# Performance work log

Measured on AMD Instinct MI355X. Metric: run time of the kernel, lower is better.

Reference implementation:

```python
import jax, jax.numpy as jnp
import numpy as np

N = 4096        # number of nodes
C = 512         # in_features
L_LAT = 64      # L_latent
EPS = 0.25      # epsilon


def setup_inputs() -> dict:
    key = jax.random.key(0)
    ks = jax.random.split(key, 8)
    def lin(k, fan_in, shape):
        return (jax.random.normal(k, shape, jnp.float32) / np.float32(np.sqrt(fan_in)))
    x = jax.random.normal(ks[0], (N, C), jnp.float32)
    adj = jax.random.uniform(ks[1], (N, N), jnp.float32)  # dense nonneg kernel
    W_proj = lin(ks[2], C, (C, L_LAT)); b_proj = jnp.zeros((L_LAT,), jnp.float32)
    W_pi1 = lin(ks[3], L_LAT, (L_LAT, C)); b_pi1 = jnp.zeros((C,), jnp.float32)
    W_pi2 = lin(ks[4], C, (C, 1)); b_pi2 = jnp.zeros((1,), jnp.float32)
    W_f = lin(ks[5], C, (C, C)); b_f = jnp.zeros((C,), jnp.float32)
    dt = jnp.array([0.1], jnp.float32)
    return {"x": x, "adj": adj, "W_proj": W_proj, "b_proj": b_proj,
            "W_pi1": W_pi1, "b_pi1": b_pi1, "W_pi2": W_pi2, "b_pi2": b_pi2,
            "W_f": W_f, "b_f": b_f, "dt": dt}


def reference(x, adj, W_proj, b_proj, W_pi1, b_pi1, W_pi2, b_pi2, W_f, b_f, dt):
    # proj_list: x -> latent [n, L]
    z = x @ W_proj + b_proj
    # pi_list: Linear -> ReLU -> Linear -> Sigmoid, squeeze to [n]
    pi = jax.nn.sigmoid(jax.nn.relu(z @ W_pi1 + b_pi1) @ W_pi2 + b_pi2)[:, 0]
    # q_epsilon_tilde: row sums of the kernel
    q = adj.sum(axis=1)                       # [n]
    # K_tilde = K_epsilon @ diag(pi/q)  == column scaling
    K_tilde = adj * (pi / q)[None, :]         # [n, n]
    # D_tilde diagonal; torch.inverse of a diagonal == elementwise reciprocal
    d = K_tilde.sum(axis=1) + 1e-5            # [n]
    # target = relu(f(x)) with f = Linear(C, C)
    target = jax.nn.relu(x @ W_f + b_f)       # [n, C]
    # L @ target = (1/eps) * diag(1/d) @ K_tilde @ target - target
    Lt = (K_tilde @ target) / (EPS * d)[:, None] - target
    return target + dt[0] * Lt
```

## Files before the change

kernel.cpp:

```cpp
#include <hip/hip_runtime.h>
#include <hip/hip_bf16.h>

#define N_NODES 4096
#define C_DIM   512
#define L_DIM   64
#define SPLITS  4
#define KCHUNK  (N_NODES / SPLITS)

typedef unsigned short u16;
typedef unsigned int   u32;
using bf16x8 = __attribute__((ext_vector_type(8))) __bf16;
using u16x8  = __attribute__((ext_vector_type(8))) unsigned short;
using f32x4  = __attribute__((ext_vector_type(4))) float;

__device__ __forceinline__ float b2f(u16 u) {
    union { unsigned int i; float f; } v; v.i = ((unsigned int)u) << 16; return v.f;
}
__device__ __forceinline__ u16 f2b(float f) {
    unsigned int u = __float_as_uint(f);
    u += 0x7fff + ((u >> 16) & 1);
    return (u16)(u >> 16);
}
__device__ __forceinline__ void gload16(const void* g, void* l) {
    __builtin_amdgcn_global_load_lds((const __attribute__((address_space(1))) void*)g,
                                     (__attribute__((address_space(3))) void*)l,
                                     16, 0, 0);
}
__device__ __forceinline__ int detect_mode_inl(const u16* __restrict__ adj) {
    int m = 0;
#pragma unroll
    for (int i = 0; i < 64; ++i) m |= (adj[i] >= 0x8000) ? 1 : 0;
    return m;
}

#define OFF_MODE  0
#define OFF_DT    64
#define OFF_BIAS  1024
#define OFF_BP    4096
#define OFF_BP1   4608
#define OFF_WP2   8192
#define OFF_BP2   10240
#define OFF_Q     16384
#define OFF_S     32768
#define OFF_DV    49152
#define OFF_WPP   65536
#define OFF_WP1P  131072
#define OFF_WFT   196608
#define OFF_T     1048576
#define OFF_TST   9437184
#define OFF_XB    13631488
#define OFF_ADJB  17825792

__device__ __forceinline__ float ldin(const void* p, int i, int mode) {
    if (mode) return ((const float*)p)[i];
    return b2f(((const u16*)p)[i]);
}

__global__ __launch_bounds__(256) void k1_prep(const void* __restrict__ adj, const void* __restrict__ x,
        const void* Wp, const void* bp, const void* Wp1, const void* bp1,
        const void* Wp2, const void* bp2, const void* Wf, const void* bfc, const void* dt,
        int* __restrict__ modep,
        float* __restrict__ bp_f, float* __restrict__ bp1_f,
        float* __restrict__ Wp2_f, float* __restrict__ bp2_f,
        float* __restrict__ bias_f, float* __restrict__ dt_f,
        u32* __restrict__ WpP, u32* __restrict__ Wp1P,
        u16* __restrict__ adjb, float* __restrict__ q, u16* __restrict__ xb,
        u16* __restrict__ WfT) {
    __shared__ float tile[32][33];
    int bid = blockIdx.x, tid = threadIdx.x;
    int mode = detect_mode_inl((const u16*)adj);
    if (bid < 7) {
        if (bid == 0 && tid == 0) *modep = mode;
        int idx = bid * 256 + tid;
        if (idx < 64)           bp_f[idx]          = ldin(bp,  idx, mode);
        else if (idx < 576)     bp1_f[idx - 64]    = ldin(bp1, idx - 64, mode);
        else if (idx < 1088)    Wp2_f[idx - 576]   = ldin(Wp2, idx - 576, mode);
        else if (idx == 1088)   bp2_f[0]           = ldin(bp2, 0, mode);
        else if (idx < 1601)    bias_f[idx - 1089] = ldin(bfc, idx - 1089, mode);
        else if (idx == 1601)   dt_f[0]            = ldin(dt, 0, mode);
    } else if (bid < 2055) {
        if (mode == 0) return;
        int idx = (bid - 7) * 256 + tid;
        float4 v = ((const float4*)x)[idx];
        ushort4 o; o.x = f2b(v.x); o.y = f2b(v.y); o.z = f2b(v.z); o.w = f2b(v.w);
        ((ushort4*)xb)[idx] = o;
    } else if (bid < 3079) {
        int wave = tid >> 6, lane = tid & 63;
        int row = (bid - 2055) * 4 + wave;
        float acc = 0.f;
        if (mode) {
            const float4* rp = (const float4*)((const float*)adj + (size_t)row * N_NODES);
            ushort4* wp = (ushort4*)(adjb + (size_t)row * N_NODES);
#pragma unroll
            for (int it = 0; it < 16; ++it) {
                float4 v = rp[it * 64 + lane];
                acc += v.x + v.y + v.z + v.w;
                ushort4 o; o.x = f2b(v.x); o.y = f2b(v.y); o.z = f2b(v.z); o.w = f2b(v.w);
                wp[it * 64 + lane] = o;
            }
        } else {
            const u16x8* rp = (const u16x8*)((const u16*)adj + (size_t)row * N_NODES);
#pragma unroll
            for (int it = 0; it < 8; ++it) {
                u16x8 v = rp[it * 64 + lane];
#pragma unroll
                for (int e = 0; e < 8; ++e) acc += b2f(v[e]);
            }
        }
#pragma unroll
        for (int off = 32; off > 0; off >>= 1) acc += __shfl_down(acc, off);
        if (lane == 0) q[row] = acc;
    } else if (bid < 3335) {
        int g = bid - 3079;
        int tx = tid & 31, ty = tid >> 5;
        int x0 = (g & 15) * 32, y0 = (g >> 4) * 32;
        if (mode) {
            const float* src = (const float*)Wf;
#pragma unroll
            for (int r = ty; r < 32; r += 8) tile[r][tx] = src[(size_t)(y0 + r) * C_DIM + x0 + tx];
        } else {
            const u16* src = (const u16*)Wf;
#pragma unroll
            for (int r = ty; r < 32; r += 8) tile[r][tx] = b2f(src[(size_t)(y0 + r) * C_DIM + x0 + tx]);
        }
        __syncthreads();
#pragma unroll
        for (int r = ty; r < 32; r += 8)
            WfT[(size_t)(x0 + r) * C_DIM + y0 + tx] = f2b(tile[tx][r]);
    } else if (bid < 3399) {
        int idx = (bid - 3335) * 256 + tid;
        int k2i = idx >> 6, j = idx & 63;
        float a = ldin(Wp, (2 * k2i) * L_DIM + j, mode);
        float b = ldin(Wp, (2 * k2i + 1) * L_DIM + j, mode);
        WpP[idx] = (u32)f2b(a) | ((u32)f2b(b) << 16);
    } else {
        int idx = (bid - 3399) * 256 + tid;
        int jj2 = idx >> 9, m = idx & 511;
        float a = ldin(Wp1, (2 * jj2) * C_DIM + m, mode);
        float b = ldin(Wp1, (2 * jj2 + 1) * C_DIM + m, mode);
        Wp1P[idx] = (u32)f2b(a) | ((u32)f2b(b) << 16);
    }
}

__global__ __launch_bounds__(256) void k2_pi_gemm1(const void* __restrict__ xraw,
        const int* __restrict__ modep, const u16* __restrict__ xb, const u16* __restrict__ WfT,
        const u32* __restrict__ WpP, const u32* __restrict__ Wp1P,
        const float* __restrict__ bp_f,  const float* __restrict__ bp1_f,
        const float* __restrict__ Wp2_f, const float* __restrict__ bp2_f,
        const float* __restrict__ bias_f, const float* __restrict__ dt_f,
        const float* __restrict__ q, float* __restrict__ s, float* __restrict__ T,
        void* __restrict__ out, float* __restrict__ Pacc) {
    __shared__ __align__(16) char smem[26880];
    int bid = blockIdx.x, tid = threadIdx.x;
    int mode = *modep;
    if (bid < 512) {
        float (*sx)[C_DIM]      = (float(*)[C_DIM])smem;
        float (*red)[8][L_DIM]  = (float(*)[8][L_DIM])(smem + 16384);
        float (*sz)[L_DIM]      = (float(*)[L_DIM])(smem + 24576);
        float (*rw)[8]          = (float(*)[8])(smem + 26624);
        int i0 = bid * 8;
        const u16* xsrc = mode ? xb : (const u16*)xraw;
        const u16x8* xp = (const u16x8*)(xsrc + (size_t)i0 * C_DIM);
#pragma unroll
        for (int r = 0; r < 2; ++r) {
            u16x8 v = xp[tid + 256 * r];
            float* dstf = &sx[0][0] + (size_t)(tid + 256 * r) * 8;
#pragma unroll
            for (int e = 0; e < 8; ++e) dstf[e] = b2f(v[e]);
        }
        __syncthreads();
        int j = tid & 63, part = tid >> 6;
        float za[8];
#pragma unroll
        for (int n = 0; n < 8; ++n) za[n] = 0.f;
        const u32* wp = WpP + part * 4096 + j;
#pragma unroll 8
        for (int kk = 0; kk < 64; ++kk) {
            u32 w = wp[kk * 64];
            float wa = b2f((u16)(w & 0xFFFF)), wb = b2f((u16)(w >> 16));
            int k = part * 128 + kk * 2;
#pragma unroll
            for (int n = 0; n < 8; ++n) za[n] += sx[n][k] * wa + sx[n][k + 1] * wb;
        }
#pragma unroll
        for (int n = 0; n < 8; ++n) red[part][n][j] = za[n];
        __syncthreads();
#pragma unroll
        for (int r = 0; r < 2; ++r) {
            int idx = tid + r * 256; int n = idx >> 6, jj = idx & 63;
            sz[n][jj] = red[0][n][jj] + red[1][n][jj] + red[2][n][jj] + red[3][n][jj] + bp_f[jj];
        }
        __syncthreads();
        int m0 = tid, m1 = tid + 256;
        float h0[8], h1[8];
        float b0 = bp1_f[m0], b1 = bp1_f[m1];
#pragma unroll
        for (int n = 0; n < 8; ++n) { h0[n] = b0; h1[n] = b1; }
        const u32* w1p = Wp1P + m0;
#pragma unroll 4
        for (int jj2 = 0; jj2 < 32; ++jj2) {
            u32 w0 = w1p[jj2 * 512], w1 = w1p[jj2 * 512 + 256];
            float w0a = b2f((u16)(w0 & 0xFFFF)), w0b = b2f((u16)(w0 >> 16));
            float w1a = b2f((u16)(w1 & 0xFFFF)), w1b = b2f((u16)(w1 >> 16));
#pragma unroll
            for (int n = 0; n < 8; ++n) {
                float za_ = sz[n][2 * jj2], zb_ = sz[n][2 * jj2 + 1];
                h0[n] += za_ * w0a + zb_ * w0b;
                h1[n] += za_ * w1a + zb_ * w1b;
            }
        }
        float w2a = Wp2_f[m0], w2b = Wp2_f[m1];
        float p[8];
#pragma unroll
        for (int n = 0; n < 8; ++n)
            p[n] = fmaxf(h0[n], 0.f) * w2a + fmaxf(h1[n], 0.f) * w2b;
#pragma unroll
        for (int off = 32; off > 0; off >>= 1)
#pragma unroll
            for (int n = 0; n < 8; ++n) p[n] += __shfl_down(p[n], off);
        int lane = tid & 63, wave = tid >> 6;
        if (lane == 0) {
#pragma unroll
            for (int n = 0; n < 8; ++n) rw[wave][n] = p[n];
        }
        __syncthreads();
        if (tid < 8) {
            float tot = rw[0][tid] + rw[1][tid] + rw[2][tid] + rw[3][tid] + bp2_f[0];
            float pi = 1.f / (1.f + expf(-tot));
            s[i0 + tid] = pi / q[i0 + tid];
        }
    } else {
        u16* lA = (u16*)smem;
        u16* lB = (u16*)(smem + 4096);
        const u16* A = mode ? xb : (const u16*)xraw;
        float* tgt = mode ? (float*)out : Pacc;
        int g = bid - 512;
        int lane = tid & 63, wave = tid >> 6;
        int bm = (g & 63) * 64, bn = (g >> 6) * 64;
        int quad = lane >> 4, l15 = lane & 15;
        int wm = wave * 16;
        const u16* Ap = A + (size_t)(bm + (tid >> 2)) * C_DIM + (tid & 3) * 8;
        const u16* Bp = WfT + (size_t)(bn + (tid >> 2)) * C_DIM + (tid & 3) * 8;
        u16* la = lA + tid * 8;
        u16* lb = lB + tid * 8;
        f32x4 acc[4];
#pragma unroll
        for (int nt = 0; nt < 4; ++nt) acc[nt] = (f32x4){0.f, 0.f, 0.f, 0.f};
        for (int k0 = 0; k0 < C_DIM; k0 += 32) {
            gload16(Ap + k0, la);
            gload16(Bp + k0, lb);
            __syncthreads();
            bf16x8 af = *(const bf16x8*)&lA[(wm + l15) * 32 + quad * 8];
            bf16x8 bfv[4];
#pragma unroll
            for (int nt = 0; nt < 4; ++nt) bfv[nt] = *(const bf16x8*)&lB[(nt * 16 + l15) * 32 + quad * 8];
#pragma unroll
            for (int nt = 0; nt < 4; ++nt)
                acc[nt] = __builtin_amdgcn_mfma_f32_16x16x32_bf16(af, bfv[nt], acc[nt], 0, 0, 0);
            __syncthreads();
        }
        float c0 = 1.f - dt_f[0];
#pragma unroll
        for (int nt = 0; nt < 4; ++nt) {
            int col = bn + nt * 16 + l15;
            float bv = bias_f[col];
#pragma unroll
            for (int r = 0; r < 4; ++r) {
                int row = bm + wm + quad * 4 + r;
                float t = fmaxf(acc[nt][r] + bv, 0.f);
                T[(size_t)row * C_DIM + col] = t;
                tgt[(size_t)row * C_DIM + col] = c0 * t;
            }
        }
    }
}

__global__ __launch_bounds__(256) void k3_mid(const void* __restrict__ adjraw,
        const int* __restrict__ modep,
        const u16* __restrict__ adjb, const float* __restrict__ s,
        const float* __restrict__ T,
        float* __restrict__ dv, u16* __restrict__ TsT) {
    __shared__ float tile[32][33];
    int bid = blockIdx.x, tid = threadIdx.x;
    int mode = *modep;
    if (bid < 1024) {
        const u16* A = mode ? adjb : (const u16*)adjraw;
        int wave = tid >> 6, lane = tid & 63;
        int row = bid * 4 + wave;
        const u16x8* rp = (const u16x8*)(A + (size_t)row * N_NODES);
        float acc = 0.f;
#pragma unroll
        for (int it = 0; it < 8; ++it) {
            int chunk = it * 64 + lane;
            u16x8 v = rp[chunk];
            const float4* sp = (const float4*)(s + chunk * 8);
            float4 s0 = sp[0], s1 = sp[1];
            acc += b2f(v[0]) * s0.x + b2f(v[1]) * s0.y + b2f(v[2]) * s0.z + b2f(v[3]) * s0.w;
            acc += b2f(v[4]) * s1.x + b2f(v[5]) * s1.y + b2f(v[6]) * s1.z + b2f(v[7]) * s1.w;
        }
#pragma unroll
        for (int off = 32; off > 0; off >>= 1) acc += __shfl_down(acc, off);
        if (lane == 0) dv[row] = acc + 1e-5f;
    } else {
        int g = bid - 1024;
        int tx = tid & 31, ty = tid >> 5;
        int x0 = (g & 15) * 32, y0 = (g >> 4) * 32;
#pragma unroll
        for (int r = ty; r < 32; r += 8) tile[r][tx] = T[(size_t)(y0 + r) * C_DIM + x0 + tx];
        __syncthreads();
        float sv = s[y0 + tx];
#pragma unroll
        for (int r = ty; r < 32; r += 8)
            TsT[(size_t)(x0 + r) * N_NODES + y0 + tx] = f2b(tile[tx][r] * sv);
    }
}

__global__ __launch_bounds__(256) void k4_gemm2(const void* __restrict__ adjraw,
        const int* __restrict__ modep,
        const u16* __restrict__ adjb, const u16* __restrict__ TsT,
        const float* __restrict__ dv, const float* __restrict__ dt_f,
        void* __restrict__ out, float* __restrict__ Pacc) {
    __shared__ __align__(16) u16 lA[8192];
    __shared__ __align__(16) u16 lB[8192];
    int mode = *modep;
    const u16* A = mode ? adjb : (const u16*)adjraw;
    float* tgt = mode ? (float*)out : Pacc;
    int tid = threadIdx.x;
    int lane = tid & 63, wave = tid >> 6;
    int bm = blockIdx.x * 128, bn = blockIdx.y * 128;
    int kbase = blockIdx.z * KCHUNK;
    int wm = (wave & 1) * 64, wn = (wave >> 1) * 64;
    int quad = lane >> 4, l15 = lane & 15;

    const u16* Ab0 = A + (size_t)(bm + (tid >> 2)) * N_NODES + kbase + (tid & 3) * 8;
    const u16* Ab1 = A + (size_t)(bm + 64 + (tid >> 2)) * N_NODES + kbase + (tid & 3) * 8;
    const u16* Bb0 = TsT + (size_t)(bn + (tid >> 2)) * N_NODES + kbase + (tid & 3) * 8;
    const u16* Bb1 = TsT + (size_t)(bn + 64 + (tid >> 2)) * N_NODES + kbase + (tid & 3) * 8;
    u16* la00 = lA + tid * 8;        u16* la01 = lA + 2048 + tid * 8;
    u16* la10 = lA + 4096 + tid * 8; u16* la11 = lA + 6144 + tid * 8;
    u16* lb00 = lB + tid * 8;        u16* lb01 = lB + 2048 + tid * 8;
    u16* lb10 = lB + 4096 + tid * 8; u16* lb11 = lB + 6144 + tid * 8;

    f32x4 acc[4][4];
#pragma unroll
    for (int a = 0; a < 4; ++a)
#pragma unroll
        for (int b = 0; b < 4; ++b) acc[a][b] = (f32x4){0.f, 0.f, 0.f, 0.f};

    for (int k0 = 0; k0 < KCHUNK; k0 += 64) {
        gload16(Ab0 + k0, la00);
        gload16(Ab1 + k0, la01);
        gload16(Ab0 + k0 + 32, la10);
        gload16(Ab1 + k0 + 32, la11);
        gload16(Bb0 + k0, lb00);
        gload16(Bb1 + k0, lb01);
        gload16(Bb0 + k0 + 32, lb10);
        gload16(Bb1 + k0 + 32, lb11);
        __syncthreads();
#pragma unroll
        for (int kk = 0; kk < 2; ++kk) {
            const u16* baseA = lA + kk * 4096;
            const u16* baseB = lB + kk * 4096;
            bf16x8 af[4], bfv[4];
#pragma unroll
            for (int mt = 0; mt < 4; ++mt) af[mt] = *(const bf16x8*)&baseA[(wm + mt * 16 + l15) * 32 + quad * 8];
#pragma unroll
            for (int nt = 0; nt < 4; ++nt) bfv[nt] = *(const bf16x8*)&baseB[(wn + nt * 16 + l15) * 32 + quad * 8];
#pragma unroll
            for (int mt = 0; mt < 4; ++mt)
#pragma unroll
                for (int nt = 0; nt < 4; ++nt)
                    acc[mt][nt] = __builtin_amdgcn_mfma_f32_16x16x32_bf16(af[mt], bfv[nt], acc[mt][nt], 0, 0, 0);
        }
        __syncthreads();
    }

    float c1 = dt_f[0] * 4.f;
#pragma unroll
    for (int mt = 0; mt < 4; ++mt) {
        float inv[4];
#pragma unroll
        for (int r = 0; r < 4; ++r) inv[r] = c1 / dv[bm + wm + mt * 16 + quad * 4 + r];
#pragma unroll
        for (int nt = 0; nt < 4; ++nt) {
            int col = bn + wn + nt * 16 + l15;
#pragma unroll
            for (int r = 0; r < 4; ++r) {
                int row = bm + wm + mt * 16 + quad * 4 + r;
                atomicAdd(&tgt[(size_t)row * C_DIM + col], acc[mt][nt][r] * inv[r]);
            }
        }
    }
}

__global__ __launch_bounds__(256) void k5_fin(const int* __restrict__ modep,
                                              const float* __restrict__ Pacc,
                                              u16* __restrict__ out) {
    if (*modep) return;
    int idx = blockIdx.x * 256 + threadIdx.x;
    float4 v = ((const float4*)Pacc)[idx];
    ushort4 o; o.x = f2b(v.x); o.y = f2b(v.y); o.z = f2b(v.z); o.w = f2b(v.w);
    ((ushort4*)out)[idx] = o;
}

extern "C" void kernel_launch(void* const* d_in, const int* in_sizes, int n_in,
                              void* d_out, int out_size, void* d_ws, size_t ws_size,
                              hipStream_t stream) {
    const void* x   = d_in[0];
    const void* adj = d_in[1];
    const void* Wp  = d_in[2];
    const void* bp  = d_in[3];
    const void* Wp1 = d_in[4];
    const void* bp1 = d_in[5];
    const void* Wp2 = d_in[6];
    const void* bp2 = d_in[7];
    const void* Wf  = d_in[8];
    const void* bfc = d_in[9];
    const void* dtp = d_in[10];

    char* ws = (char*)d_ws;
    int*   modep  = (int*)(ws + OFF_MODE);
    float* dt_f   = (float*)(ws + OFF_DT);
    float* bias_f = (float*)(ws + OFF_BIAS);
    float* bp_f   = (float*)(ws + OFF_BP);
    float* bp1_f  = (float*)(ws + OFF_BP1);
    float* Wp2_f  = (float*)(ws + OFF_WP2);
    float* bp2_f  = (float*)(ws + OFF_BP2);
    float* q      = (float*)(ws + OFF_Q);
    float* s      = (float*)(ws + OFF_S);
    float* dv     = (float*)(ws + OFF_DV);
    u32*   WpP    = (u32*)(ws + OFF_WPP);
    u32*   Wp1P   = (u32*)(ws + OFF_WP1P);
    u16*   WfT    = (u16*)(ws + OFF_WFT);
    float* T      = (float*)(ws + OFF_T);
    u16*   TsT    = (u16*)(ws + OFF_TST);
    u16*   xb     = (u16*)(ws + OFF_XB);
    u16*   adjb   = (u16*)(ws + OFF_ADJB);
    float* Pacc   = (float*)(ws + OFF_ADJB);

    k1_prep<<<3463, 256, 0, stream>>>(adj, x, Wp, bp, Wp1, bp1, Wp2, bp2, Wf, bfc, dtp,
                                      modep, bp_f, bp1_f, Wp2_f, bp2_f, bias_f, dt_f,
                                      WpP, Wp1P, adjb, q, xb, WfT);
    k2_pi_gemm1<<<1024, 256, 0, stream>>>(x, modep, xb, WfT, WpP, Wp1P,
                                          bp_f, bp1_f, Wp2_f, bp2_f, bias_f, dt_f,
                                          q, s, T, d_out, Pacc);
    k3_mid<<<3072, 256, 0, stream>>>(adj, modep, adjb, s, T, dv, TsT);
    k4_gemm2<<<dim3(32, 4, SPLITS), 256, 0, stream>>>(adj, modep, adjb, TsT, dv, dt_f, d_out, Pacc);
    k5_fin<<<2048, 256, 0, stream>>>(modep, Pacc, (u16*)d_out);
}
```

Measured before the change: 215.4 us.

## Fuse target GEMM with scaled transpose, double-buffer GEMM loads, reorder prep blocks

Splits the pi MLP into its own kernel and moves the x@Wf GEMM into the mid kernel. Its epilogue now writes the s-scaled, transposed bf16 target directly from LDS, which removes the fp32 T intermediate and the separate transpose pass. Both MFMA GEMMs gain double-buffered LDS staging, with explicit vmcnt waits and barriers replacing per-step syncthreads so loads overlap compute. The prep kernel puts the adjacency row-sum/convert blocks first, and f2b now uses the native bf16 cast. In exchange, the GEMM kernel uses twice the LDS, and the hand-written waitcnt and barrier sequence must be correct.

Result: no change. 218.6 us (+1.5%).

```diff
diff --git a/kernel.cpp b/kernel.cpp
--- a/kernel.cpp
+++ b/kernel.cpp
@@ -17,9 +17,8 @@
     union { unsigned int i; float f; } v; v.i = ((unsigned int)u) << 16; return v.f;
 }
 __device__ __forceinline__ u16 f2b(float f) {
-    unsigned int u = __float_as_uint(f);
-    u += 0x7fff + ((u >> 16) & 1);
-    return (u16)(u >> 16);
+    __bf16 h = (__bf16)f;
+    union { __bf16 h; u16 u; } v; v.h = h; return v.u;
 }
 __device__ __forceinline__ void gload16(const void* g, void* l) {
     __builtin_amdgcn_global_load_lds((const __attribute__((address_space(1))) void*)g,
@@ -31,6 +30,10 @@
 #pragma unroll
     for (int i = 0; i < 64; ++i) m |= (adj[i] >= 0x8000) ? 1 : 0;
     return m;
+}
+__device__ __forceinline__ float ldin(const void* p, int i, int mode) {
+    if (mode) return ((const float*)p)[i];
+    return b2f(((const u16*)p)[i]);
 }
 
 #define OFF_MODE  0
@@ -46,15 +49,9 @@
 #define OFF_WPP   65536
 #define OFF_WP1P  131072
 #define OFF_WFT   196608
-#define OFF_T     1048576
 #define OFF_TST   9437184
 #define OFF_XB    13631488
 #define OFF_ADJB  17825792
-
-__device__ __forceinline__ float ldin(const void* p, int i, int mode) {
-    if (mode) return ((const float*)p)[i];
-    return b2f(((const u16*)p)[i]);
-}
 
 __global__ __launch_bounds__(256) void k1_prep(const void* __restrict__ adj, const void* __restrict__ x,
         const void* Wp, const void* bp, const void* Wp1, const void* bp1,
@@ -69,221 +66,179 @@
     __shared__ float tile[32][33];
     int bid = blockIdx.x, tid = threadIdx.x;
     int mode = detect_mode_inl((const u16*)adj);
-    if (bid < 7) {
-        if (bid == 0 && tid == 0) *modep = mode;
-        int idx = bid * 256 + tid;
+    if (bid < 1024) {
+        int wave = tid >> 6, lane = tid & 63;
+        int row = bid * 4 + wave;
+        float acc = 0.f;
+        if (mode) {
+            const float4* rp = (const float4*)((const float*)adj + (size_t)row * N_NODES);
+            ushort4* wp = (ushort4*)(adjb + (size_t)row * N_NODES);
+#pragma unroll 8
+            for (int it = 0; it < 16; ++it) {
+                float4 v = rp[it * 64 + lane];
+                acc += (v.x + v.y) + (v.z + v.w);
+                ushort4 o; o.x = f2b(v.x); o.y = f2b(v.y); o.z = f2b(v.z); o.w = f2b(v.w);
+                wp[it * 64 + lane] = o;
+            }
+        } else {
+            const u16x8* rp = (const u16x8*)((const u16*)adj + (size_t)row * N_NODES);
+#pragma unroll
+            for (int it = 0; it < 8; ++it) {
+                u16x8 v = rp[it * 64 + lane];
+#pragma unroll
+                for (int e = 0; e < 8; ++e) acc += b2f(v[e]);
+            }
+        }
+#pragma unroll
+        for (int off = 32; off > 0; off >>= 1) acc += __shfl_down(acc, off);
+        if (lane == 0) q[row] = acc;
+    } else if (bid < 3072) {
+        if (mode == 0) return;
+        int idx = (bid - 1024) * 256 + tid;
+        float4 v = ((const float4*)x)[idx];
+        ushort4 o; o.x = f2b(v.x); o.y = f2b(v.y); o.z = f2b(v.z); o.w = f2b(v.w);
+        ((ushort4*)xb)[idx] = o;
+    } else if (bid < 3328) {
+        int g = bid - 3072;
+        int tx = tid & 31, ty = tid >> 5;
+        int x0 = (g & 15) * 32, y0 = (g >> 4) * 32;
+        if (mode) {
+            const float* src = (const float*)Wf;
+#pragma unroll
+            for (int r = ty; r < 32; r += 8) tile[r][tx] = src[(size_t)(y0 + r) * C_DIM + x0 + tx];
+        } else {
+            const u16* src = (const u16*)Wf;
+#pragma unroll
+            for (int r = ty; r < 32; r += 8) tile[r][tx] = b2f(src[(size_t)(y0 + r) * C_DIM + x0 + tx]);
+        }
+        __syncthreads();
+#pragma unroll
+        for (int r = ty; r < 32; r += 8)
+            WfT[(size_t)(x0 + r) * C_DIM + y0 + tx] = f2b(tile[tx][r]);
+    } else if (bid < 3392) {
+        int idx = (bid - 3328) * 256 + tid;
+        int k2i = idx >> 6, j = idx & 63;
+        float a = ldin(Wp, (2 * k2i) * L_DIM + j, mode);
+        float b = ldin(Wp, (2 * k2i + 1) * L_DIM + j, mode);
+        WpP[idx] = (u32)f2b(a) | ((u32)f2b(b) << 16);
+    } else if (bid < 3456) {
+        int idx = (bid - 3392) * 256 + tid;
+        int jj2 = idx >> 9, m = idx & 511;
+        float a = ldin(Wp1, (2 * jj2) * C_DIM + m, mode);
+        float b = ldin(Wp1, (2 * jj2 + 1) * C_DIM + m, mode);
+        Wp1P[idx] = (u32)f2b(a) | ((u32)f2b(b) << 16);
+    } else {
+        if (bid == 3456 && tid == 0) *modep = mode;
+        int idx = (bid - 3456) * 256 + tid;
         if (idx < 64)           bp_f[idx]          = ldin(bp,  idx, mode);
         else if (idx < 576)     bp1_f[idx - 64]    = ldin(bp1, idx - 64, mode);
         else if (idx < 1088)    Wp2_f[idx - 576]   = ldin(Wp2, idx - 576, mode);
         else if (idx == 1088)   bp2_f[0]           = ldin(bp2, 0, mode);
         else if (idx < 1601)    bias_f[idx - 1089] = ldin(bfc, idx - 1089, mode);
         else if (idx == 1601)   dt_f[0]            = ldin(dt, 0, mode);
-    } else if (bid < 2055) {
-        if (mode == 0) return;
-        int idx = (bid - 7) * 256 + tid;
-        float4 v = ((const float4*)x)[idx];
-        ushort4 o; o.x = f2b(v.x); o.y = f2b(v.y); o.z = f2b(v.z); o.w = f2b(v.w);
-        ((ushort4*)xb)[idx] = o;
-    } else if (bid < 3079) {
-        int wave = tid >> 6, lane = tid & 63;
-        int row = (bid - 2055) * 4 + wave;
-        float acc = 0.f;
-        if (mode) {
-            const float4* rp = (const float4*)((const float*)adj + (size_t)row * N_NODES);
-            ushort4* wp = (ushort4*)(adjb + (size_t)row * N_NODES);
-#pragma unroll
-            for (int it = 0; it < 16; ++it) {
-                float4 v = rp[it * 64 + lane];
-                acc += v.x + v.y + v.z + v.w;
-                ushort4 o; o.x = f2b(v.x); o.y = f2b(v.y); o.z = f2b(v.z); o.w = f2b(v.w);
-                wp[it * 64 + lane] = o;
-            }
-        } else {
-            const u16x8* rp = (const u16x8*)((const u16*)adj + (size_t)row * N_NODES);
-#pragma unroll
-            for (int it = 0; it < 8; ++it) {
-                u16x8 v = rp[it * 64 + lane];
-#pragma unroll
-                for (int e = 0; e < 8; ++e) acc += b2f(v[e]);
-            }
-        }
-#pragma unroll
-        for (int off = 32; off > 0; off >>= 1) acc += __shfl_down(acc, off);
-        if (lane == 0) q[row] = acc;
-    } else if (bid < 3335) {
-        int g = bid - 3079;
-        int tx = tid & 31, ty = tid >> 5;
-        int x0 = (g & 15) * 32, y0 = (g >> 4) * 32;
-        if (mode) {
-            const float* src = (const float*)Wf;
-#pragma unroll
-            for (int r = ty; r < 32; r += 8) tile[r][tx] = src[(size_t)(y0 + r) * C_DIM + x0 + tx];
-        } else {
-            const u16* src = (const u16*)Wf;
-#pragma unroll
-            for (int r = ty; r < 32; r += 8) tile[r][tx] = b2f(src[(size_t)(y0 + r) * C_DIM + x0 + tx]);
-        }
-        __syncthreads();
-#pragma unroll
-        for (int r = ty; r < 32; r += 8)
-            WfT[(size_t)(x0 + r) * C_DIM + y0 + tx] = f2b(tile[tx][r]);
-    } else if (bid < 3399) {
-        int idx = (bid - 3335) * 256 + tid;
-        int k2i = idx >> 6, j = idx & 63;
-        float a = ldin(Wp, (2 * k2i) * L_DIM + j, mode);
-        float b = ldin(Wp, (2 * k2i + 1) * L_DIM + j, mode);
-        WpP[idx] = (u32)f2b(a) | ((u32)f2b(b) << 16);
-    } else {
-        int idx = (bid - 3399) * 256 + tid;
-        int jj2 = idx >> 9, m = idx & 511;
-        float a = ldin(Wp1, (2 * jj2) * C_DIM + m, mode);
-        float b = ldin(Wp1, (2 * jj2 + 1) * C_DIM + m, mode);
-        Wp1P[idx] = (u32)f2b(a) | ((u32)f2b(b) << 16);
-    }
-}
-
-__global__ __launch_bounds__(256) void k2_pi_gemm1(const void* __restrict__ xraw,
-        const int* __restrict__ modep, const u16* __restrict__ xb, const u16* __restrict__ WfT,
+    }
+}
+
+__global__ __launch_bounds__(256) void k1p_pi(const void* __restrict__ xraw,
+        const int* __restrict__ modep, const u16* __restrict__ xb,
         const u32* __restrict__ WpP, const u32* __restrict__ Wp1P,
         const float* __restrict__ bp_f,  const float* __restrict__ bp1_f,
         const float* __restrict__ Wp2_f, const float* __restrict__ bp2_f,
-        const float* __restrict__ bias_f, const float* __restrict__ dt_f,
-        const float* __restrict__ q, float* __restrict__ s, float* __restrict__ T,
-        void* __restrict__ out, float* __restrict__ Pacc) {
+        const float* __restrict__ q, float* __restrict__ s) {
     __shared__ __align__(16) char smem[26880];
     int bid = blockIdx.x, tid = threadIdx.x;
     int mode = *modep;
-    if (bid < 512) {
-        float (*sx)[C_DIM]      = (float(*)[C_DIM])smem;
-        float (*red)[8][L_DIM]  = (float(*)[8][L_DIM])(smem + 16384);
-        float (*sz)[L_DIM]      = (float(*)[L_DIM])(smem + 24576);
-        float (*rw)[8]          = (float(*)[8])(smem + 26624);
-        int i0 = bid * 8;
-        const u16* xsrc = mode ? xb : (const u16*)xraw;
-        const u16x8* xp = (const u16x8*)(xsrc + (size_t)i0 * C_DIM);
-#pragma unroll
-        for (int r = 0; r < 2; ++r) {
-            u16x8 v = xp[tid + 256 * r];
-            float* dstf = &sx[0][0] + (size_t)(tid + 256 * r) * 8;
-#pragma unroll
-            for (int e = 0; e < 8; ++e) dstf[e] = b2f(v[e]);
-        }
-        __syncthreads();
-        int j = tid & 63, part = tid >> 6;
-        float za[8];
-#pragma unroll
-        for (int n = 0; n < 8; ++n) za[n] = 0.f;
-        const u32* wp = WpP + part * 4096 + j;
+    float (*sx)[C_DIM]      = (float(*)[C_DIM])smem;
+    float (*red)[8][L_DIM]  = (float(*)[8][L_DIM])(smem + 16384);
+    float (*sz)[L_DIM]      = (float(*)[L_DIM])(smem + 24576);
+    float (*rw)[8]          = (float(*)[8])(smem + 26624);
+    int i0 = bid * 8;
+    const u16* xsrc = mode ? xb : (const u16*)xraw;
+    const u16x8* xp = (const u16x8*)(xsrc + (size_t)i0 * C_DIM);
+#pragma unroll
+    for (int r = 0; r < 2; ++r) {
+        u16x8 v = xp[tid + 256 * r];
+        float* dstf = &sx[0][0] + (size_t)(tid + 256 * r) * 8;
+#pragma unroll
+        for (int e = 0; e < 8; ++e) dstf[e] = b2f(v[e]);
+    }
+    __syncthreads();
+    int j = tid & 63, part = tid >> 6;
+    float za[8];
+#pragma unroll
+    for (int n = 0; n < 8; ++n) za[n] = 0.f;
+    const u32* wp = WpP + part * 4096 + j;
 #pragma unroll 8
-        for (int kk = 0; kk < 64; ++kk) {
-            u32 w = wp[kk * 64];
-            float wa = b2f((u16)(w & 0xFFFF)), wb = b2f((u16)(w >> 16));
-            int k = part * 128 + kk * 2;
-#pragma unroll
-            for (int n = 0; n < 8; ++n) za[n] += sx[n][k] * wa + sx[n][k + 1] * wb;
-        }
-#pragma unroll
-        for (int n = 0; n < 8; ++n) red[part][n][j] = za[n];
-        __syncthreads();
-#pragma unroll
-        for (int r = 0; r < 2; ++r) {
-            int idx = tid + r * 256; int n = idx >> 6, jj = idx & 63;
-            sz[n][jj] = red[0][n][jj] + red[1][n][jj] + red[2][n][jj] + red[3][n][jj] + bp_f[jj];
-        }
-        __syncthreads();
-        int m0 = tid, m1 = tid + 256;
-        float h0[8], h1[8];
-        float b0 = bp1_f[m0], b1 = bp1_f[m1];
-#pragma unroll
-        for (int n = 0; n < 8; ++n) { h0[n] = b0; h1[n] = b1; }
-        const u32* w1p = Wp1P + m0;
+    for (int kk = 0; kk < 64; ++kk) {
+        u32 w = wp[kk * 64];
+        float wa = b2f((u16)(w & 0xFFFF)), wb = b2f((u16)(w >> 16));
+        int k = part * 128 + kk * 2;
+#pragma unroll
+        for (int n = 0; n < 8; ++n) za[n] += sx[n][k] * wa + sx[n][k + 1] * wb;
+    }
+#pragma unroll
+    for (int n = 0; n < 8; ++n) red[part][n][j] = za[n];
+    __syncthreads();
+#pragma unroll
+    for (int r = 0; r < 2; ++r) {
+        int idx = tid + r * 256; int n = idx >> 6, jj = idx & 63;
+        sz[n][jj] = red[0][n][jj] + red[1][n][jj] + red[2][n][jj] + red[3][n][jj] + bp_f[jj];
+    }
+    __syncthreads();
+    int m0 = tid, m1 = tid + 256;
+    float h0[8], h1[8];
+    float b0 = bp1_f[m0], b1 = bp1_f[m1];
+#pragma unroll
+    for (int n = 0; n < 8; ++n) { h0[n] = b0; h1[n] = b1; }
+    const u32* w1p = Wp1P + m0;
 #pragma unroll 4
-        for (int jj2 = 0; jj2 < 32; ++jj2) {
-            u32 w0 = w1p[jj2 * 512], w1 = w1p[jj2 * 512 + 256];
-            float w0a = b2f((u16)(w0 & 0xFFFF)), w0b = b2f((u16)(w0 >> 16));
-            float w1a = b2f((u16)(w1 & 0xFFFF)), w1b = b2f((u16)(w1 >> 16));
-#pragma unroll
-            for (int n = 0; n < 8; ++n) {
-                float za_ = sz[n][2 * jj2], zb_ = sz[n][2 * jj2 + 1];
-                h0[n] += za_ * w0a + zb_ * w0b;
-                h1[n] += za_ * w1a + zb_ * w1b;
-            }
-        }
-        float w2a = Wp2_f[m0], w2b = Wp2_f[m1];
-        float p[8];
-#pragma unroll
-        for (int n = 0; n < 8; ++n)
-            p[n] = fmaxf(h0[n], 0.f) * w2a + fmaxf(h1[n], 0.f) * w2b;
-#pragma unroll
-        for (int off = 32; off > 0; off >>= 1)
-#pragma unroll
-            for (int n = 0; n < 8; ++n) p[n] += __shfl_down(p[n], off);
-        int lane = tid & 63, wave = tid >> 6;
-        if (lane == 0) {
-#pragma unroll
-            for (int n = 0; n < 8; ++n) rw[wave][n] = p[n];
-        }
-        __syncthreads();
-        if (tid < 8) {
-            float tot = rw[0][tid] + rw[1][tid] + rw[2][tid] + rw[3][tid] + bp2_f[0];
-            float pi = 1.f / (1.f + expf(-tot));
-            s[i0 + tid] = pi / q[i0 + tid];
-        }
-    } else {
-        u16* lA = (u16*)smem;
-        u16* lB = (u16*)(smem + 4096);
-        const u16* A = mode ? xb : (const u16*)xraw;
-        float* tgt = mode ? (float*)out : Pacc;
-        int g = bid - 512;
-        int lane = tid & 63, wave = tid >> 6;
-        int bm = (g & 63) * 64, bn = (g >> 6) * 64;
-        int quad = lane >> 4, l15 = lane & 15;
-        int wm = wave * 16;
-        const u16* Ap = A + (size_t)(bm + (tid >> 2)) * C_DIM + (tid & 3) * 8;
-        const u16* Bp = WfT + (size_t)(bn + (tid >> 2)) * C_DIM + (tid & 3) * 8;
-        u16* la = lA + tid * 8;
-        u16* lb = lB + tid * 8;
-        f32x4 acc[4];
-#pragma unroll
-        for (int nt = 0; nt < 4; ++nt) acc[nt] = (f32x4){0.f, 0.f, 0.f, 0.f};
-        for (int k0 = 0; k0 < C_DIM; k0 += 32) {
-            gload16(Ap + k0, la);
-            gload16(Bp + k0, lb);
-            __syncthreads();
-            bf16x8 af = *(const bf16x8*)&lA[(wm + l15) * 32 + quad * 8];
-            bf16x8 bfv[4];
-#pragma unroll
-            for (int nt = 0; nt < 4; ++nt) bfv[nt] = *(const bf16x8*)&lB[(nt * 16 + l15) * 32 + quad * 8];
-#pragma unroll
-            for (int nt = 0; nt < 4; ++nt)
-                acc[nt] = __builtin_amdgcn_mfma_f32_16x16x32_bf16(af, bfv[nt], acc[nt], 0, 0, 0);
-            __syncthreads();
-        }
-        float c0 = 1.f - dt_f[0];
-#pragma unroll
-        for (int nt = 0; nt < 4; ++nt) {
-            int col = bn + nt * 16 + l15;
-            float bv = bias_f[col];
-#pragma unroll
-            for (int r = 0; r < 4; ++r) {
-                int row = bm + wm + quad * 4 + r;
-                float t = fmaxf(acc[nt][r] + bv, 0.f);
-                T[(size_t)row * C_DIM + col] = t;
-                tgt[(size_t)row * C_DIM + col] = c0 * t;
-            }
-        }
-    }
-}
-
-__global__ __launch_bounds__(256) void k3_mid(const void* __restrict__ adjraw,
+    for (int jj2 = 0; jj2 < 32; ++jj2) {
+        u32 w0 = w1p[jj2 * 512], w1 = w1p[jj2 * 512 + 256];
+        float w0a = b2f((u16)(w0 & 0xFFFF)), w0b = b2f((u16)(w0 >> 16));
+        float w1a = b2f((u16)(w1 & 0xFFFF)), w1b = b2f((u16)(w1 >> 16));
+#pragma unroll
+        for (int n = 0; n < 8; ++n) {
+            float za_ = sz[n][2 * jj2], zb_ = sz[n][2 * jj2 + 1];
+            h0[n] += za_ * w0a + zb_ * w0b;
+            h1[n] += za_ * w1a + zb_ * w1b;
+        }
+    }
+    float w2a = Wp2_f[m0], w2b = Wp2_f[m1];
+    float p[8];
+#pragma unroll
+    for (int n = 0; n < 8; ++n)
+        p[n] = fmaxf(h0[n], 0.f) * w2a + fmaxf(h1[n], 0.f) * w2b;
+#pragma unroll
+    for (int off = 32; off > 0; off >>= 1)
+#pragma unroll
+        for (int n = 0; n < 8; ++n) p[n] += __shfl_down(p[n], off);
+    int lane = tid & 63, wave = tid >> 6;
+    if (lane == 0) {
+#pragma unroll
+        for (int n = 0; n < 8; ++n) rw[wave][n] = p[n];
+    }
+    __syncthreads();
+    if (tid < 8) {
+        float tot = rw[0][tid] + rw[1][tid] + rw[2][tid] + rw[3][tid] + bp2_f[0];
+        float pi = 1.f / (1.f + expf(-tot));
+        s[i0 + tid] = pi / q[i0 + tid];
+    }
+}
+
+__global__ __launch_bounds__(256) void k2_mid(const void* __restrict__ adjraw, const void* __restrict__ xraw,
         const int* __restrict__ modep,
-        const u16* __restrict__ adjb, const float* __restrict__ s,
-        const float* __restrict__ T,
-        float* __restrict__ dv, u16* __restrict__ TsT) {
-    __shared__ float tile[32][33];
+        const float* __restrict__ s, const float* __restrict__ bias_f, const float* __restrict__ dt_f,
+        const u16* __restrict__ adjb, const u16* __restrict__ xb, const u16* __restrict__ WfT,
+        float* __restrict__ dv, u16* __restrict__ TsT,
+        void* __restrict__ out, float* __restrict__ Pacc) {
+    __shared__ __align__(16) char smem[16640];
     int bid = blockIdx.x, tid = threadIdx.x;
     int mode = *modep;
     if (bid < 1024) {
+        float* s_lds = (float*)smem;
+#pragma unroll
+        for (int r = 0; r < 4; ++r) ((float4*)s_lds)[tid + 256 * r] = ((const float4*)s)[tid + 256 * r];
+        __syncthreads();
         const u16* A = mode ? adjb : (const u16*)adjraw;
         int wave = tid >> 6, lane = tid & 63;
         int row = bid * 4 + wave;
@@ -293,7 +248,7 @@
         for (int it = 0; it < 8; ++it) {
             int chunk = it * 64 + lane;
             u16x8 v = rp[chunk];
-            const float4* sp = (const float4*)(s + chunk * 8);
+            const float4* sp = (const float4*)(s_lds + chunk * 8);
             float4 s0 = sp[0], s1 = sp[1];
             acc += b2f(v[0]) * s0.x + b2f(v[1]) * s0.y + b2f(v[2]) * s0.z + b2f(v[3]) * s0.w;
             acc += b2f(v[4]) * s1.x + b2f(v[5]) * s1.y + b2f(v[6]) * s1.z + b2f(v[7]) * s1.w;
@@ -302,26 +257,78 @@
         for (int off = 32; off > 0; off >>= 1) acc += __shfl_down(acc, off);
         if (lane == 0) dv[row] = acc + 1e-5f;
     } else {
+        u16* lbuf = (u16*)smem;
+        u16* lT = (u16*)smem;
+        float* s_row = (float*)(smem + 16384);
         int g = bid - 1024;
-        int tx = tid & 31, ty = tid >> 5;
-        int x0 = (g & 15) * 32, y0 = (g >> 4) * 32;
-#pragma unroll
-        for (int r = ty; r < 32; r += 8) tile[r][tx] = T[(size_t)(y0 + r) * C_DIM + x0 + tx];
+        int lane = tid & 63, wave = tid >> 6;
+        int bm = (g & 63) * 64, bn = (g >> 6) * 64;
+        if (tid < 64) s_row[tid] = s[bm + tid];
+        const u16* A = mode ? xb : (const u16*)xraw;
+        float* tgt = mode ? (float*)out : Pacc;
+        int quad = lane >> 4, l15 = lane & 15;
+        int wm = wave * 16;
+        const u16* Ap = A + (size_t)(bm + (tid >> 2)) * C_DIM + (tid & 3) * 8;
+        const u16* Bp = WfT + (size_t)(bn + (tid >> 2)) * C_DIM + (tid & 3) * 8;
+        f32x4 acc[4];
+#pragma unroll
+        for (int nt = 0; nt < 4; ++nt) acc[nt] = (f32x4){0.f, 0.f, 0.f, 0.f};
+#define STAGE1(buf, k0)                                        \
+        do {                                                   \
+            gload16(Ap + (k0), lbuf + (buf) * 2048 + tid * 8); \
+            gload16(Bp + (k0), lbuf + 4096 + (buf) * 2048 + tid * 8); \
+        } while (0)
+        STAGE1(0, 0);
+        for (int it = 0; it < 16; ++it) {
+            int cur = it & 1;
+            if (it < 15) {
+                STAGE1(cur ^ 1, (it + 1) * 32);
+                asm volatile("s_waitcnt vmcnt(2)\n\ts_barrier" ::: "memory");
+            } else {
+                asm volatile("s_waitcnt vmcnt(0)\n\ts_barrier" ::: "memory");
+            }
+            __builtin_amdgcn_sched_barrier(0);
+            bf16x8 af = *(const bf16x8*)&lbuf[cur * 2048 + (wm + l15) * 32 + quad * 8];
+            bf16x8 bfv[4];
+#pragma unroll
+            for (int nt = 0; nt < 4; ++nt)
+                bfv[nt] = *(const bf16x8*)&lbuf[4096 + cur * 2048 + (nt * 16 + l15) * 32 + quad * 8];
+#pragma unroll
+            for (int nt = 0; nt < 4; ++nt)
+                acc[nt] = __builtin_amdgcn_mfma_f32_16x16x32_bf16(af, bfv[nt], acc[nt], 0, 0, 0);
+            asm volatile("s_waitcnt lgkmcnt(0)\n\ts_barrier" ::: "memory");
+        }
+#undef STAGE1
+        float c0 = 1.f - dt_f[0];
+#pragma unroll
+        for (int nt = 0; nt < 4; ++nt) {
+            int col_l = nt * 16 + l15;
+            float bv = bias_f[bn + col_l];
+#pragma unroll
+            for (int r = 0; r < 4; ++r) {
+                int row_l = wm + quad * 4 + r;
+                float t = fmaxf(acc[nt][r] + bv, 0.f);
+                tgt[(size_t)(bm + row_l) * C_DIM + bn + col_l] = c0 * t;
+                lT[col_l * 64 + row_l] = f2b(t * s_row[row_l]);
+            }
+        }
         __syncthreads();
-        float sv = s[y0 + tx];
-#pragma unroll
-        for (int r = ty; r < 32; r += 8)
-            TsT[(size_t)(x0 + r) * N_NODES + y0 + tx] = f2b(tile[tx][r] * sv);
-    }
-}
-
-__global__ __launch_bounds__(256) void k4_gemm2(const void* __restrict__ adjraw,
+        int col_l = tid >> 2, seg = tid & 3;
+        uint4 w0 = *(const uint4*)&lT[col_l * 64 + seg * 16];
+        uint4 w1 = *(const uint4*)&lT[col_l * 64 + seg * 16 + 8];
+        u16* dst = TsT + (size_t)(bn + col_l) * N_NODES + bm + seg * 16;
+        *(uint4*)dst = w0;
+        *(uint4*)(dst + 8) = w1;
+    }
+}
+
+__global__ __launch_bounds__(256) void k3_gemm2(const void* __restrict__ adjraw,
         const int* __restrict__ modep,
         const u16* __restrict__ adjb, const u16* __restrict__ TsT,
         const float* __restrict__ dv, const float* __restrict__ dt_f,
         void* __restrict__ out, float* __restrict__ Pacc) {
-    __shared__ __align__(16) u16 lA[8192];
-    __shared__ __align__(16) u16 lB[8192];
+    __shared__ __align__(16) u16 lA[2][8192];
+    __shared__ __align__(16) u16 lB[2][8192];
     int mode = *modep;
     const u16* A = mode ? adjb : (const u16*)adjraw;
     float* tgt = mode ? (float*)out : Pacc;
@@ -336,10 +343,6 @@
     const u16* Ab1 = A + (size_t)(bm + 64 + (tid >> 2)) * N_NODES + kbase + (tid & 3) * 8;
     const u16* Bb0 = TsT + (size_t)(bn + (tid >> 2)) * N_NODES + kbase + (tid & 3) * 8;
     const u16* Bb1 = TsT + (size_t)(bn + 64 + (tid >> 2)) * N_NODES + kbase + (tid & 3) * 8;
-    u16* la00 = lA + tid * 8;        u16* la01 = lA + 2048 + tid * 8;
-    u16* la10 = lA + 4096 + tid * 8; u16* la11 = lA + 6144 + tid * 8;
-    u16* lb00 = lB + tid * 8;        u16* lb01 = lB + 2048 + tid * 8;
-    u16* lb10 = lB + 4096 + tid * 8; u16* lb11 = lB + 6144 + tid * 8;
 
     f32x4 acc[4][4];
 #pragma unroll
@@ -347,20 +350,34 @@
 #pragma unroll
         for (int b = 0; b < 4; ++b) acc[a][b] = (f32x4){0.f, 0.f, 0.f, 0.f};
 
-    for (int k0 = 0; k0 < KCHUNK; k0 += 64) {
-        gload16(Ab0 + k0, la00);
-        gload16(Ab1 + k0, la01);
-        gload16(Ab0 + k0 + 32, la10);
-        gload16(Ab1 + k0 + 32, la11);
-        gload16(Bb0 + k0, lb00);
-        gload16(Bb1 + k0, lb01);
-        gload16(Bb0 + k0 + 32, lb10);
-        gload16(Bb1 + k0 + 32, lb11);
-        __syncthreads();
+#define STAGE(buf, k0)                                        \
+    do {                                                      \
+        u16* bA = &lA[(buf)][0];                              \
+        u16* bB = &lB[(buf)][0];                              \
+        gload16(Ab0 + (k0),      bA + tid * 8);               \
+        gload16(Ab1 + (k0),      bA + 2048 + tid * 8);        \
+        gload16(Ab0 + (k0) + 32, bA + 4096 + tid * 8);        \
+        gload16(Ab1 + (k0) + 32, bA + 6144 + tid * 8);        \
+        gload16(Bb0 + (k0),      bB + tid * 8);               \
+        gload16(Bb1 + (k0),      bB + 2048 + tid * 8);        \
+        gload16(Bb0 + (k0) + 32, bB + 4096 + tid * 8);        \
+        gload16(Bb1 + (k0) + 32, bB + 6144 + tid * 8);        \
+    } while (0)
+
+    STAGE(0, 0);
+    for (int it = 0; it < 16; ++it) {
+        int cur = it & 1;
+        if (it < 15) {
+            STAGE(cur ^ 1, (it + 1) * 64);
+            asm volatile("s_waitcnt vmcnt(8)\n\ts_barrier" ::: "memory");
+        } else {
+            asm volatile("s_waitcnt vmcnt(0)\n\ts_barrier" ::: "memory");
+        }
+        __builtin_amdgcn_sched_barrier(0);
 #pragma unroll
         for (int kk = 0; kk < 2; ++kk) {
-            const u16* baseA = lA + kk * 4096;
-            const u16* baseB = lB + kk * 4096;
+            const u16* baseA = &lA[cur][kk * 4096];
+            const u16* baseB = &lB[cur][kk * 4096];
             bf16x8 af[4], bfv[4];
 #pragma unroll
             for (int mt = 0; mt < 4; ++mt) af[mt] = *(const bf16x8*)&baseA[(wm + mt * 16 + l15) * 32 + quad * 8];
@@ -372,8 +389,9 @@
                 for (int nt = 0; nt < 4; ++nt)
                     acc[mt][nt] = __builtin_amdgcn_mfma_f32_16x16x32_bf16(af[mt], bfv[nt], acc[mt][nt], 0, 0, 0);
         }
-        __syncthreads();
-    }
+        asm volatile("s_waitcnt lgkmcnt(0)\n\ts_barrier" ::: "memory");
+    }
+#undef STAGE
 
     float c1 = dt_f[0] * 4.f;
 #pragma unroll
@@ -432,7 +450,6 @@
     u32*   WpP    = (u32*)(ws + OFF_WPP);
     u32*   Wp1P   = (u32*)(ws + OFF_WP1P);
     u16*   WfT    = (u16*)(ws + OFF_WFT);
-    float* T      = (float*)(ws + OFF_T);
     u16*   TsT    = (u16*)(ws + OFF_TST);
     u16*   xb     = (u16*)(ws + OFF_XB);
     u16*   adjb   = (u16*)(ws + OFF_ADJB);
@@ -441,10 +458,9 @@
     k1_prep<<<3463, 256, 0, stream>>>(adj, x, Wp, bp, Wp1, bp1, Wp2, bp2, Wf, bfc, dtp,
                                       modep, bp_f, bp1_f, Wp2_f, bp2_f, bias_f, dt_f,
                                       WpP, Wp1P, adjb, q, xb, WfT);
-    k2_pi_gemm1<<<1024, 256, 0, stream>>>(x, modep, xb, WfT, WpP, Wp1P,
-                                          bp_f, bp1_f, Wp2_f, bp2_f, bias_f, dt_f,
-                                          q, s, T, d_out, Pacc);
-    k3_mid<<<3072, 256, 0, stream>>>(adj, modep, adjb, s, T, dv, TsT);
-    k4_gemm2<<<dim3(32, 4, SPLITS), 256, 0, stream>>>(adj, modep, adjb, TsT, dv, dt_f, d_out, Pacc);
+    k1p_pi<<<512, 256, 0, stream>>>(x, modep, xb, WpP, Wp1P, bp_f, bp1_f, Wp2_f, bp2_f, q, s);
+    k2_mid<<<1536, 256, 0, stream>>>(adj, x, modep, s, bias_f, dt_f, adjb, xb, WfT,
+                                     dv, TsT, d_out, Pacc);
+    k3_gemm2<<<dim3(32, 4, SPLITS), 256, 0, stream>>>(adj, modep, adjb, TsT, dv, dt_f, d_out, Pacc);
     k5_fin<<<2048, 256, 0, stream>>>(modep, Pacc, (u16*)d_out);
 }
```
